# Optimization experiments

Hardware: AMD Instinct MI355X
Metric: run time of the kernel (lower is better)

## Reference

```python
import jax, jax.numpy as jnp
import numpy as np

B, IN_C, OUT_C, K, Z_DIM = 32, 128, 128, 3, 512
H, W, STRIDE = 56, 56, 1


def setup_inputs() -> dict:
    key = jax.random.key(0)
    k1, k2, k3 = jax.random.split(key, 3)
    x = jax.random.normal(k1, (B, IN_C, H, W), dtype=jnp.float32)
    z = jax.random.normal(k2, (B, Z_DIM), dtype=jnp.float32)
    # nn.Linear(z_dim, out_c*in_c*k*k): weight [out_f, in_f], bias [out_f]
    out_f = OUT_C * IN_C * K * K
    W_head = jax.random.normal(k3, (out_f, Z_DIM), dtype=jnp.float32) * (1.0 / np.sqrt(Z_DIM))
    b_head = jnp.zeros((out_f,), dtype=jnp.float32)
    return {"x": x, "z": z, "W_head": W_head, "b_head": b_head}


def reference(x, z, W_head, b_head):
    b = x.shape[0]
    # hypernetwork head: per-sample conv weights
    w = z @ W_head.T + b_head                       # [B, out_c*in_c*k*k]
    w = w.reshape(b, OUT_C, IN_C, K, K)             # [B, O, I, K, K]

    pad = K // 2

    def conv_one(xi, wi):
        # xi: [I, H, W], wi: [O, I, K, K] -> [O, H', W']
        out = jax.lax.conv_general_dilated(
            xi[None],                                # [1, I, H, W]
            wi,
            window_strides=(STRIDE, STRIDE),
            padding=[(pad, pad), (pad, pad)],
            dimension_numbers=("NCHW", "OIHW", "NCHW"),
        )
        return out[0]

    return jax.vmap(conv_one)(x, w)                 # [B, O, H', W']
```

## Files before the change

kernel.cpp:

```cpp
#include <hip/hip_runtime.h>
#include <hip/hip_bf16.h>
#include <stdint.h>

#define BB 32
#define IC 128
#define OC 128
#define HH 56
#define WW 56
#define ZD 512
#define NRS 9
#define OI (OC*IC)
#define WROWS (OI*NRS)
#define WDIM 58
#define NHEADBLK (WROWS / 64)
#define NTRBLK (HH * BB)

typedef float  f32x4  __attribute__((ext_vector_type(4)));
typedef short  bf16x8 __attribute__((ext_vector_type(8)));

static __device__ __forceinline__ short f2bf(float f) {
    uint32_t u = __float_as_uint(f);
    uint32_t r = (u + 0x7fffu + ((u >> 16) & 1u)) >> 16;
    return (short)r;
}
static __device__ __forceinline__ short f2bf_hw(float f) {
    __hip_bfloat16 h = __float2bfloat16(f);
    return *reinterpret_cast<short*>(&h);
}
static __device__ __forceinline__ float bf2f(short s) {
    uint32_t u = ((uint32_t)(uint16_t)s) << 16;
    return __uint_as_float(u);
}
static __device__ __forceinline__ void gll16(const void* g, void* l) {
    __builtin_amdgcn_global_load_lds(
        (const __attribute__((address_space(1))) uint32_t*)g,
        (__attribute__((address_space(3))) uint32_t*)l, 16, 0, 0);
}

__global__ __launch_bounds__(256, 2) void fused_head_tr_kernel(
    const float* __restrict__ Wh, const float* __restrict__ z,
    short* __restrict__ wnat,
    const float* __restrict__ x, short* __restrict__ xt)
{
    if (blockIdx.x >= NHEADBLK) {
        const int bx = blockIdx.x - NHEADBLK;
        const int b = bx / HH;
        const int h = bx - b * HH;
        const int w = threadIdx.x & 63;
        const int yq = threadIdx.x >> 6;
        if (w >= WW) return;
        const float* xp = x + (size_t)b * IC * HH * WW + h * WW + w;
        short* op = xt + (((size_t)(b * HH + h)) * WW + w) * IC;
        #pragma unroll
        for (int q = 0; q < 4; ++q) {
            int ic = yq * 4 + q;
            bf16x8 pk;
            #pragma unroll
            for (int j = 0; j < 8; ++j) {
                float v = xp[(size_t)(ic * 8 + j) * (HH * WW)];
                pk[j] = f2bf(v);
            }
            *(bf16x8*)(op + ic * 8) = pk;
        }
        return;
    }

    __shared__ __align__(16) char Zl[32 * 1024];
    const int tid  = threadIdx.x;
    const int lane = tid & 63;
    const int wv   = tid >> 6;

    {
        const int b = tid >> 3, ks = (tid & 7) * 64;
        const float* zp = z + (size_t)b * ZD + ks;
        const int bx = (b & 7) << 4;
        #pragma unroll
        for (int j8 = 0; j8 < 8; ++j8) {
            f32x4 v0 = *(const f32x4*)(zp + j8 * 8);
            f32x4 v1 = *(const f32x4*)(zp + j8 * 8 + 4);
            bf16x8 pk;
            pk[0] = f2bf_hw(v0.x); pk[1] = f2bf_hw(v0.y);
            pk[2] = f2bf_hw(v0.z); pk[3] = f2bf_hw(v0.w);
            pk[4] = f2bf_hw(v1.x); pk[5] = f2bf_hw(v1.y);
            pk[6] = f2bf_hw(v1.z); pk[7] = f2bf_hw(v1.w);
            *(bf16x8*)(Zl + b * 1024 + ((ks * 2 + j8 * 16) ^ bx)) = pk;
        }
    }
    __syncthreads();

    const int rl = lane & 15;
    const int kq = lane >> 4;
    const int zxor = (rl & 7) << 4;
    const int rowg = blockIdx.x * 64 + wv * 16 + rl;

    const char* wp = (const char*)Wh + (size_t)rowg * (ZD * 4) + kq * 32;

    f32x4 wd[32];
    #pragma unroll
    for (int i = 0; i < 16; ++i) {
        wd[2 * i]     = *(const f32x4*)(wp + i * 128);
        wd[2 * i + 1] = *(const f32x4*)(wp + i * 128 + 16);
    }

    f32x4 acc0 = {0.f, 0.f, 0.f, 0.f}, acc1 = {0.f, 0.f, 0.f, 0.f};
    #pragma unroll
    for (int kb = 0; kb < 16; ++kb) {
        const int koff = (kb * 64 + kq * 16) ^ zxor;
        bf16x8 a0 = *(const bf16x8*)(Zl + rl * 1024 + koff);
        bf16x8 a1 = *(const bf16x8*)(Zl + (16 + rl) * 1024 + koff);
        f32x4 lo = wd[2 * kb];
        f32x4 hi = wd[2 * kb + 1];
        bf16x8 bw;
        bw[0] = f2bf_hw(lo.x); bw[1] = f2bf_hw(lo.y);
        bw[2] = f2bf_hw(lo.z); bw[3] = f2bf_hw(lo.w);
        bw[4] = f2bf_hw(hi.x); bw[5] = f2bf_hw(hi.y);
        bw[6] = f2bf_hw(hi.z); bw[7] = f2bf_hw(hi.w);
        acc0 = __builtin_amdgcn_mfma_f32_16x16x32_bf16(a0, bw, acc0, 0, 0, 0);
        acc1 = __builtin_amdgcn_mfma_f32_16x16x32_bf16(a1, bw, acc1, 0, 0, 0);
    }

    #pragma unroll
    for (int reg = 0; reg < 4; ++reg) {
        const int b0 = kq * 4 + reg;
        wnat[(size_t)b0 * WROWS + rowg]        = f2bf(acc0[reg]);
        wnat[(size_t)(16 + b0) * WROWS + rowg] = f2bf(acc1[reg]);
    }
}

__global__ __launch_bounds__(256) void repack_kernel(
    const short* __restrict__ wnat, const float* __restrict__ bh,
    short* __restrict__ wbf)
{
    const int b = blockIdx.y;
    const int oi0 = blockIdx.x * 2048 + threadIdx.x * 8;
    const short* src = wnat + (size_t)b * WROWS + (size_t)oi0 * 9;
    const float* bp  = bh + (size_t)oi0 * 9;

    bf16x8 in[9];
    #pragma unroll
    for (int j = 0; j < 9; ++j) in[j] = *(const bf16x8*)(src + j * 8);
    f32x4 bv[18];
    #pragma unroll
    for (int m = 0; m < 18; ++m) bv[m] = *(const f32x4*)(bp + m * 4);

    #pragma unroll
    for (int rs = 0; rs < 9; ++rs) {
        bf16x8 o;
        #pragma unroll
        for (int jj = 0; jj < 8; ++jj) {
            const int e = jj * 9 + rs;
            float v = bf2f(in[e >> 3][e & 7]) + bv[e >> 2][e & 3];
            o[jj] = f2bf(v);
        }
        *(bf16x8*)(wbf + ((size_t)(b * 9 + rs)) * OI + oi0) = o;
    }
}

__global__ __launch_bounds__(256) void conv_kernel(
    const short* __restrict__ wbf,
    const short* __restrict__ xt,
    float* __restrict__ out)
{
    __shared__ __align__(16) char Xl[3 * WDIM * 256];
    __shared__ __align__(16) char Wl[128 * 256];
    const int tid  = threadIdx.x;
    const int lane = tid & 63;
    const int wv   = tid >> 6;
    const int h = blockIdx.x;
    const int b = blockIdx.y;

    #pragma unroll
    for (int q = 0; q < 11; ++q) {
        int idx = tid + q * 256;
        if (idx < 3 * WDIM * 16) ((f32x4*)Xl)[idx] = (f32x4){0.f, 0.f, 0.f, 0.f};
    }
    __syncthreads();

    for (int r = 0; r < 3; ++r) {
        int hin = h + r - 1;
        if (hin < 0 || hin >= HH) continue;
        const char* src = (const char*)(xt + ((size_t)(b * HH + hin)) * WW * IC);
        char* dstbase = Xl + (r * WDIM + 1) * 256;
        for (int it = wv; it < 14; it += 4) {
            int c = it * 64 + lane;
            int u = r * WDIM + 1 + (c >> 4);
            int soff = (c * 16) ^ ((u & 7) << 4);
            gll16(src + soff, dstbase + it * 1024);
        }
    }

    f32x4 acc[2][4];
    #pragma unroll
    for (int a = 0; a < 2; ++a)
        #pragma unroll
        for (int p = 0; p < 4; ++p) acc[a][p] = (f32x4){0.f, 0.f, 0.f, 0.f};

    const int axor = (lane & 7) << 4;
    int kkoff[4];
    #pragma unroll
    for (int kk = 0; kk < 4; ++kk) kkoff[kk] = kk * 64 + ((lane >> 4) << 4);

    for (int rs = 0; rs < 9; ++rs) {
        __syncthreads();
        const char* wsrc = (const char*)(wbf + ((size_t)b * NRS + rs) * OI);
        for (int it = wv; it < 32; it += 4) {
            int c = it * 64 + lane;
            int soff = (c * 16) ^ (((c >> 4) & 7) << 4);
            gll16(wsrc + soff, Wl + it * 1024);
        }
        __syncthreads();

        const int r = rs / 3, s = rs - 3 * (rs / 3);
        int ubase[4], bswz[4];
        #pragma unroll
        for (int pf = 0; pf < 4; ++pf) {
            int p = pf * 16 + (lane & 15);
            int pc = p > 55 ? 55 : p;
            int uu = r * WDIM + pc + s;
            ubase[pf] = uu * 256;
            bswz[pf] = (uu & 7) << 4;
        }
        #pragma unroll
        for (int kk = 0; kk < 4; ++kk) {
            bf16x8 a0 = *(const bf16x8*)(Wl + (wv * 32 + (lane & 15)) * 256 +
                                         (kkoff[kk] ^ axor));
            bf16x8 a1 = *(const bf16x8*)(Wl + (wv * 32 + 16 + (lane & 15)) * 256 +
                                         (kkoff[kk] ^ axor));
            #pragma unroll
            for (int pf = 0; pf < 4; ++pf) {
                bf16x8 bv = *(const bf16x8*)(Xl + ubase[pf] + (kkoff[kk] ^ bswz[pf]));
                acc[0][pf] = __builtin_amdgcn_mfma_f32_16x16x32_bf16(a0, bv, acc[0][pf], 0, 0, 0);
                acc[1][pf] = __builtin_amdgcn_mfma_f32_16x16x32_bf16(a1, bv, acc[1][pf], 0, 0, 0);
            }
        }
    }

    const int pcol = lane & 15;
    const int rowq = lane >> 4;
    #pragma unroll
    for (int a = 0; a < 2; ++a) {
        int o0 = wv * 32 + a * 16 + rowq * 4;
        #pragma unroll
        for (int pf = 0; pf < 4; ++pf) {
            int p = pf * 16 + pcol;
            if (p < WW) {
                #pragma unroll
                for (int reg = 0; reg < 4; ++reg) {
                    out[(((size_t)b * OC + (o0 + reg)) * HH + h) * WW + p] = acc[a][pf][reg];
                }
            }
        }
    }
}

extern "C" void kernel_launch(void* const* d_in, const int* in_sizes, int n_in,
                              void* d_out, int out_size, void* d_ws, size_t ws_size,
                              hipStream_t stream) {
    const float* x  = (const float*)d_in[0];
    const float* z  = (const float*)d_in[1];
    const float* Wh = (const float*)d_in[2];
    const float* bh = (const float*)d_in[3];
    float* out = (float*)d_out;

    short* wnat = (short*)d_ws;
    short* wbf  = (short*)((char*)d_ws + 9437184);
    short* xt   = (short*)((char*)d_ws + 18874368);

    fused_head_tr_kernel<<<dim3(NHEADBLK + NTRBLK), 256, 0, stream>>>(Wh, z, wnat, x, xt);
    repack_kernel<<<dim3(8, 32), 256, 0, stream>>>(wnat, bh, wbf);
    transpose_kernel_dummy:;
    conv_kernel<<<dim3(HH, BB), 256, 0, stream>>>(wbf, xt, out);
}
```

Measured before the change: 164.1 us.

## Compute two output rows per conv block with triple-buffered weight prefetch

The conv kernel now uses 512 threads, and each block computes two adjacent output rows. The 4-row input tile is shared, so every per-sample weight slice loaded into LDS serves twice as many MFMAs. Weight loading moves to a triple-buffered asynchronous pipeline: the next rs slice is issued before the current one is computed, with one barrier per step instead of two. This raises LDS use to about 155 KB per block and halves the grid, which may cut occupancy and reduce the number of blocks in flight.

```diff
diff --git a/kernel.cpp b/kernel.cpp
--- a/kernel.cpp
+++ b/kernel.cpp
@@ -14,6 +14,7 @@
 #define WDIM 58
 #define NHEADBLK (WROWS / 64)
 #define NTRBLK (HH * BB)
+#define XTILE (4 * WDIM * 256)
 
 typedef float  f32x4  __attribute__((ext_vector_type(4)));
 typedef short  bf16x8 __attribute__((ext_vector_type(8)));
@@ -156,38 +157,54 @@
     }
 }
 
-__global__ __launch_bounds__(256) void conv_kernel(
+__global__ __launch_bounds__(512) void conv_kernel(
     const short* __restrict__ wbf,
     const short* __restrict__ xt,
     float* __restrict__ out)
 {
-    __shared__ __align__(16) char Xl[3 * WDIM * 256];
-    __shared__ __align__(16) char Wl[128 * 256];
+    __shared__ __align__(16) char Xl[XTILE];
+    __shared__ __align__(16) char Wl[3][32768];
     const int tid  = threadIdx.x;
     const int lane = tid & 63;
     const int wv   = tid >> 6;
-    const int h = blockIdx.x;
-    const int b = blockIdx.y;
-
-    #pragma unroll
-    for (int q = 0; q < 11; ++q) {
-        int idx = tid + q * 256;
-        if (idx < 3 * WDIM * 16) ((f32x4*)Xl)[idx] = (f32x4){0.f, 0.f, 0.f, 0.f};
+    const int og   = wv & 3;
+    const int hh   = wv >> 2;
+    const int h0 = blockIdx.x * 2;
+    const int b  = blockIdx.y;
+
+    #pragma unroll
+    for (int q = 0; q < 8; ++q) {
+        int idx = tid + q * 512;
+        if (idx < XTILE / 16) ((f32x4*)Xl)[idx] = (f32x4){0.f, 0.f, 0.f, 0.f};
     }
     __syncthreads();
 
-    for (int r = 0; r < 3; ++r) {
-        int hin = h + r - 1;
+    for (int r = 0; r < 4; ++r) {
+        int hin = h0 + r - 1;
         if (hin < 0 || hin >= HH) continue;
         const char* src = (const char*)(xt + ((size_t)(b * HH + hin)) * WW * IC);
-        char* dstbase = Xl + (r * WDIM + 1) * 256;
-        for (int it = wv; it < 14; it += 4) {
+        char* dstb = Xl + (r * WDIM + 1) * 256;
+        for (int it = wv; it < 14; it += 8) {
             int c = it * 64 + lane;
             int u = r * WDIM + 1 + (c >> 4);
             int soff = (c * 16) ^ ((u & 7) << 4);
-            gll16(src + soff, dstbase + it * 1024);
-        }
-    }
+            gll16(src + soff, dstb + it * 1024);
+        }
+    }
+
+    #define STAGE_CW(rs_, buf_)                                                 \
+        {                                                                       \
+            const char* ws_ = (const char*)(wbf +                               \
+                ((size_t)b * NRS + (rs_)) * OI);                                \
+            _Pragma("unroll")                                                   \
+            for (int it_ = 0; it_ < 4; ++it_) {                                 \
+                int c_ = (wv * 4 + it_) * 64 + lane;                            \
+                int so_ = (c_ * 16) ^ (((c_ >> 4) & 7) << 4);                   \
+                gll16(ws_ + so_, Wl[buf_] + (wv * 4 + it_) * 1024);             \
+            }                                                                   \
+        }
+
+    STAGE_CW(0, 0);
 
     f32x4 acc[2][4];
     #pragma unroll
@@ -201,30 +218,29 @@
     for (int kk = 0; kk < 4; ++kk) kkoff[kk] = kk * 64 + ((lane >> 4) << 4);
 
     for (int rs = 0; rs < 9; ++rs) {
-        __syncthreads();
-        const char* wsrc = (const char*)(wbf + ((size_t)b * NRS + rs) * OI);
-        for (int it = wv; it < 32; it += 4) {
-            int c = it * 64 + lane;
-            int soff = (c * 16) ^ (((c >> 4) & 7) << 4);
-            gll16(wsrc + soff, Wl + it * 1024);
-        }
-        __syncthreads();
-
-        const int r = rs / 3, s = rs - 3 * (rs / 3);
+        if (rs < 8) STAGE_CW(rs + 1, (rs + 1) % 3);
+        if (rs == 8) { asm volatile("s_waitcnt vmcnt(0)" ::: "memory"); }
+        else         { asm volatile("s_waitcnt vmcnt(4)" ::: "memory"); }
+        __builtin_amdgcn_sched_barrier(0);
+        __builtin_amdgcn_s_barrier();
+        __builtin_amdgcn_sched_barrier(0);
+
+        const char* Wb = Wl[rs % 3];
+        const int r = rs / 3, s = rs - 3 * r;
         int ubase[4], bswz[4];
         #pragma unroll
         for (int pf = 0; pf < 4; ++pf) {
             int p = pf * 16 + (lane & 15);
             int pc = p > 55 ? 55 : p;
-            int uu = r * WDIM + pc + s;
+            int uu = (hh + r) * WDIM + pc + s;
             ubase[pf] = uu * 256;
             bswz[pf] = (uu & 7) << 4;
         }
         #pragma unroll
         for (int kk = 0; kk < 4; ++kk) {
-            bf16x8 a0 = *(const bf16x8*)(Wl + (wv * 32 + (lane & 15)) * 256 +
+            bf16x8 a0 = *(const bf16x8*)(Wb + (og * 32 + (lane & 15)) * 256 +
                                          (kkoff[kk] ^ axor));
-            bf16x8 a1 = *(const bf16x8*)(Wl + (wv * 32 + 16 + (lane & 15)) * 256 +
+            bf16x8 a1 = *(const bf16x8*)(Wb + (og * 32 + 16 + (lane & 15)) * 256 +
                                          (kkoff[kk] ^ axor));
             #pragma unroll
             for (int pf = 0; pf < 4; ++pf) {
@@ -234,19 +250,21 @@
             }
         }
     }
+    #undef STAGE_CW
 
     const int pcol = lane & 15;
     const int rowq = lane >> 4;
-    #pragma unroll
-    for (int a = 0; a < 2; ++a) {
-        int o0 = wv * 32 + a * 16 + rowq * 4;
+    const int hO = h0 + hh;
+    #pragma unroll
+    for (int aa = 0; aa < 2; ++aa) {
+        int o0 = og * 32 + aa * 16 + rowq * 4;
         #pragma unroll
         for (int pf = 0; pf < 4; ++pf) {
             int p = pf * 16 + pcol;
             if (p < WW) {
                 #pragma unroll
                 for (int reg = 0; reg < 4; ++reg) {
-                    out[(((size_t)b * OC + (o0 + reg)) * HH + h) * WW + p] = acc[a][pf][reg];
+                    out[(((size_t)b * OC + (o0 + reg)) * HH + hO) * WW + p] = acc[aa][pf][reg];
                 }
             }
         }
@@ -268,6 +286,5 @@
 
     fused_head_tr_kernel<<<dim3(NHEADBLK + NTRBLK), 256, 0, stream>>>(Wh, z, wnat, x, xt);
     repack_kernel<<<dim3(8, 32), 256, 0, stream>>>(wnat, bh, wbf);
-    transpose_kernel_dummy:;
-    conv_kernel<<<dim3(HH, BB), 256, 0, stream>>>(wbf, xt, out);
-}
+    conv_kernel<<<dim3(HH / 2, BB), 512, 0, stream>>>(wbf, xt, out);
+}
```

Measured after the change: 158.1 us. 3.6% less time.
